# Kernel tuning notes

Hardware: AMD Instinct MI355X
Metric: run time of the kernel (lower is better)

The kernel has to match this reference:

```python
import jax, jax.numpy as jnp
import numpy as np

B, NB, D, H = 2048, 12, 256, 16
NU, NI, NR = 100000, 100000, 6
EPS = 1e-10


def _lin(k, din, dout):
    k1, k2 = jax.random.split(k)
    s = 1.0 / np.sqrt(din)
    w = jax.random.uniform(k1, (din, dout), minval=-s, maxval=s, dtype=jnp.float32)
    b = jax.random.uniform(k2, (dout,), minval=-s, maxval=s, dtype=jnp.float32)
    return w, b


def setup_inputs() -> dict:
    key = jax.random.key(0)
    ks = jax.random.split(key, 24)
    inp = {}
    inp['iids'] = jax.random.randint(ks[0], (B,), 0, NI)
    inp['i_user_pad'] = jnp.stack([
        jax.random.randint(ks[1], (B, NB), 0, NU),
        jax.random.randint(ks[2], (B, NB), 0, NR)], axis=-1)
    inp['i_item_pad'] = jax.random.randint(ks[3], (B, NB), 0, NI)
    inp['i_item_user_pad'] = jnp.stack([
        jax.random.randint(ks[4], (B, NB, NB), 0, NI),
        jax.random.randint(ks[5], (B, NB, NB), 0, NR)], axis=-1)
    inp['user_table'] = jax.random.normal(ks[6], (NU, D), dtype=jnp.float32) * 0.02
    inp['item_table'] = jax.random.normal(ks[7], (NI, D), dtype=jnp.float32) * 0.02
    inp['rate_table'] = jax.random.normal(ks[8], (NR, D), dtype=jnp.float32) * 0.02
    # g_u: 2D -> D -> D
    inp['g_u_w1'], inp['g_u_b1'] = _lin(ks[9], 2 * D, D)
    inp['g_u_w2'], inp['g_u_b2'] = _lin(ks[10], D, D)
    # item_users_att: 2D -> D -> H
    inp['attu_w1'], inp['attu_b1'] = _lin(ks[11], 2 * D, D)
    inp['attu_w2'], inp['attu_b2'] = _lin(ks[12], D, H)
    # item_users_head: NB*H -> NB*H//2 -> NB
    inp['headu_w1'], inp['headu_b1'] = _lin(ks[13], NB * H, NB * H // 2)
    inp['headu_w2'], inp['headu_b2'] = _lin(ks[14], NB * H // 2, NB)
    # aggre_items: D -> D (+relu)
    inp['aggi_w'], inp['aggi_b'] = _lin(ks[15], D, D)
    # item_items_att: 2D -> D -> H
    inp['attii_w1'], inp['attii_b1'] = _lin(ks[16], 2 * D, D)
    inp['attii_w2'], inp['attii_b2'] = _lin(ks[17], D, H)
    # item_items_head: NB*H -> NB*H//2 -> NB
    inp['headii_w1'], inp['headii_b1'] = _lin(ks[18], NB * H, NB * H // 2)
    inp['headii_w2'], inp['headii_b2'] = _lin(ks[19], NB * H // 2, NB)
    # aggre_item2item: D -> D (+relu)
    inp['aggii_w'], inp['aggii_b'] = _lin(ks[20], D, D)
    # combine_mlp: 2D -> D -> D -> D, relu each
    inp['comb_w1'], inp['comb_b1'] = _lin(ks[21], 2 * D, D)
    inp['comb_w2'], inp['comb_b2'] = _lin(ks[22], D, D)
    inp['comb_w3'], inp['comb_b3'] = _lin(ks[23], D, D)
    return inp


def _mlp(x, w1, b1, w2, b2):
    return jax.nn.relu(x @ w1 + b1) @ w2 + b2


def reference(iids, i_user_pad, i_item_pad, i_item_user_pad,
              user_table, item_table, rate_table,
              g_u_w1, g_u_b1, g_u_w2, g_u_b2,
              attu_w1, attu_b1, attu_w2, attu_b2,
              headu_w1, headu_b1, headu_w2, headu_b2,
              aggi_w, aggi_b,
              attii_w1, attii_b1, attii_w2, attii_b2,
              headii_w1, headii_b1, headii_w2, headii_b2,
              aggii_w, aggii_b,
              comb_w1, comb_b1, comb_w2, comb_b2, comb_w3, comb_b3):
    dt = user_table.dtype
    # ---- stage 1: item <- its users ----
    p_t = user_table[i_user_pad[:, :, 0]]                       # [B,NB,D]
    mask_i = (i_user_pad[:, :, 0] > 0).astype(dt)               # [B,NB]
    er = rate_table[i_user_pad[:, :, 1]]                        # [B,NB,D]
    f_jt = _mlp(jnp.concatenate([p_t, er], -1), g_u_w1, g_u_b1, g_u_w2, g_u_b2)
    q_j = mask_i[:, :, None] * item_table[iids][:, None, :]     # [B,NB,D]
    miu = _mlp(jnp.concatenate([f_jt, q_j], -1), attu_w1, attu_b1, attu_w2, attu_b2)  # [B,NB,H]
    miu = _mlp(miu.reshape(miu.shape[0], -1), headu_w1, headu_b1, headu_w2, headu_b2)  # [B,NB]
    miu = jnp.exp(miu) * mask_i
    miu = miu / (jnp.sum(miu, 1, keepdims=True) + EPS)
    h_jU = jax.nn.relu(jnp.einsum('bn,bnd->bd', miu, f_jt) @ aggi_w + aggi_b)
    # ---- stage 2: neighbor items <- their users ----
    q_a_s = item_table[i_item_user_pad[..., 0]]                 # [B,NB,NB,D]
    mask_s = (i_item_user_pad[..., 0] > 0).astype(dt)           # [B,NB,NB]
    er_s = rate_table[i_item_user_pad[..., 1]]
    x_ia_s = _mlp(jnp.concatenate([q_a_s, er_s], -1), g_u_w1, g_u_b1, g_u_w2, g_u_b2)
    p_i_s = mask_s[..., None] * item_table[i_item_pad][:, :, None, :]
    miu_s = _mlp(jnp.concatenate([x_ia_s, p_i_s], -1), attu_w1, attu_b1, attu_w2, attu_b2)  # [B,NB,NB,H]
    miu_s = _mlp(miu_s.reshape(miu_s.shape[0], miu_s.shape[1], -1),
                 headu_w1, headu_b1, headu_w2, headu_b2)        # [B,NB,NB]
    miu_s = jnp.exp(miu_s) * mask_s
    miu_s = miu_s / (jnp.sum(miu_s, 2, keepdims=True) + EPS)
    h_oU = jax.nn.relu(jnp.einsum('bnm,bnmd->bnd', miu_s, x_ia_s) @ aggi_w + aggi_b)  # [B,NB,D]
    # ---- stage 3: item <- neighbor items ----
    kappa = _mlp(jnp.concatenate([h_oU, item_table[i_item_pad]], -1),
                 attii_w1, attii_b1, attii_w2, attii_b2)        # [B,NB,H]
    kappa = _mlp(kappa.reshape(kappa.shape[0], -1), headii_w1, headii_b1, headii_w2, headii_b2)  # [B,NB]
    mask_su = (i_item_pad > 0).astype(dt)
    kappa = jnp.exp(kappa) * mask_su
    kappa = kappa / (jnp.sum(kappa, 1, keepdims=True) + EPS)
    h_jV = jax.nn.relu(jnp.einsum('bn,bnd->bd', kappa, h_oU) @ aggii_w + aggii_b)
    # ---- combine ----
    h = jnp.concatenate([h_jU, h_jV], 1)
    h = jax.nn.relu(h @ comb_w1 + comb_b1)
    h = jax.nn.relu(h @ comb_w2 + comb_b2)
    return jax.nn.relu(h @ comb_w3 + comb_b3)
```

## Files before the change

### kernel.cpp

```cpp
#include <hip/hip_runtime.h>
#include <cstdint>
#include <cstddef>

typedef short short8 __attribute__((ext_vector_type(8)));
typedef short short4v __attribute__((ext_vector_type(4)));
typedef float f32x4 __attribute__((ext_vector_type(4)));
typedef __bf16 bf16x8 __attribute__((ext_vector_type(8)));

__device__ __forceinline__ unsigned short f2bu(float f) {
  return __builtin_bit_cast(unsigned short, (__bf16)f);
}
__device__ __forceinline__ float b2f(unsigned short h) {
  union { unsigned u; float f; } v; v.u = ((unsigned)h) << 16;
  return v.f;
}

__device__ __forceinline__ f32x4 mfma16(short8 a, short8 b, f32x4 c) {
  return __builtin_amdgcn_mfma_f32_16x16x32_bf16(
      __builtin_bit_cast(bf16x8, a), __builtin_bit_cast(bf16x8, b), c, 0, 0, 0);
}

__global__ void k_cvt(const float* __restrict__ in, short* __restrict__ o, int ntot) {
  int i = (blockIdx.x * 256 + threadIdx.x) * 8;
  if (i >= ntot) return;
  float4 a = *(const float4*)(in + i);
  float4 b = *(const float4*)(in + i + 4);
  short8 v;
  v[0] = (short)f2bu(a.x); v[1] = (short)f2bu(a.y);
  v[2] = (short)f2bu(a.z); v[3] = (short)f2bu(a.w);
  v[4] = (short)f2bu(b.x); v[5] = (short)f2bu(b.y);
  v[6] = (short)f2bu(b.z); v[7] = (short)f2bu(b.w);
  *(short8*)(o + i) = v;
}

__global__ void k_cvt_rows(const float* __restrict__ tab, const int* __restrict__ pairs,
                           short* __restrict__ o, int nrows) {
  int t = blockIdx.x * 256 + threadIdx.x;
  if (t >= nrows * 32) return;
  int row = t >> 5;
  int c8 = (t & 31) << 3;
  int id = pairs[2 * row];
  const float* s = tab + (size_t)id * 256 + c8;
  float4 a = *(const float4*)(s);
  float4 b = *(const float4*)(s + 4);
  short8 v;
  v[0] = (short)f2bu(a.x); v[1] = (short)f2bu(a.y);
  v[2] = (short)f2bu(a.z); v[3] = (short)f2bu(a.w);
  v[4] = (short)f2bu(b.x); v[5] = (short)f2bu(b.y);
  v[6] = (short)f2bu(b.z); v[7] = (short)f2bu(b.w);
  *(short8*)(o + (size_t)row * 256 + c8) = v;
}

struct Prep {
  const float* src[16];
  short* dst[16];
  int K[16], N[16], mode[16];
  int boff[17];
};
__global__ void k_prep(Prep p) {
  int b = blockIdx.x, e = 0;
#pragma unroll
  for (int i = 1; i < 16; ++i) if (b >= p.boff[i]) e = i;
  int t = (b - p.boff[e]) * 256 + threadIdx.x;
  const int K = p.K[e], N = p.N[e];
  if (t >= K * N) return;
  const float* w = p.src[e];
  const int m = p.mode[e];
  if (m == 2) { p.dst[e][t] = (short)f2bu(w[t]); return; }
  if (m == 0) {
    int ks = t >> 13, rem = t & 8191;
    int P = rem >> 3, j = rem & 7;
    int n = P >> 2;
    int kq = ((P & 3) - (n >> 1)) & 3;
    int k = (ks << 5) + (kq << 3) + j;
    p.dst[e][t] = (short)f2bu(w[(size_t)k * 256 + n]);
    return;
  }
  int n = t / K, k = t - n * K;
  p.dst[e][t] = (short)f2bu(w[(size_t)k * N + n]);
}

__global__ void k_rc(const float* __restrict__ rate, const float* __restrict__ w1,
                     float* __restrict__ RC) {
  const int j = blockIdx.x;
  const int n = threadIdx.x;
  float s = 0.f;
  const float* rr = rate + j * 256;
  for (int k = 0; k < 256; ++k)
    s += rr[k] * w1[(size_t)(256 + k) * 256 + n];
  RC[j * 256 + n] = s;
}

__global__ __launch_bounds__(256, 4) void k_qc(
    const int* __restrict__ qid, const short* __restrict__ itembf,
    const short* __restrict__ aw1, float* __restrict__ QC)
{
  const int tid = threadIdx.x;
  const int lane = tid & 63;
  const int wave = tid >> 6;
  const int m0 = (int)blockIdx.x << 6;
  const int l15 = lane & 15;
  const int lq = lane >> 4;
  const int nb = wave << 6;

  int pBg[4];
  const short* qp[4];
#pragma unroll
  for (int i = 0; i < 4; ++i) {
    int n = nb + i * 16 + l15;
    pBg[i] = (n * 4 + ((lq + (n >> 1)) & 3)) * 8;
    qp[i] = itembf + (size_t)qid[m0 + i * 16 + l15] * 256 + lq * 8;
  }

  const f32x4 fz = {0.f, 0.f, 0.f, 0.f};
  f32x4 acc[4][4];
#pragma unroll
  for (int ni = 0; ni < 4; ++ni)
#pragma unroll
    for (int mi = 0; mi < 4; ++mi) acc[ni][mi] = fz;

  for (int ks = 0; ks < 8; ++ks) {
    short8 wf[4], qf[4];
#pragma unroll
    for (int i = 0; i < 4; ++i) {
      wf[i] = *(const short8*)(aw1 + (8 + ks) * 8192 + pBg[i]);
      qf[i] = *(const short8*)(qp[i] + ks * 32);
    }
#pragma unroll
    for (int ni = 0; ni < 4; ++ni)
#pragma unroll
      for (int mi = 0; mi < 4; ++mi)
        acc[ni][mi] = mfma16(wf[ni], qf[mi], acc[ni][mi]);
  }
#pragma unroll
  for (int ni = 0; ni < 4; ++ni) {
    const int nbase = nb + ni * 16 + lq * 4;
#pragma unroll
    for (int mi = 0; mi < 4; ++mi) {
      const int m = mi * 16 + l15;
      *(f32x4*)(QC + (size_t)(m0 + m) * 256 + nbase) = acc[ni][mi];
    }
  }
}

template <bool IDENT>
__global__ __launch_bounds__(256, 3) void k_fused(
    const int* __restrict__ idx_pairs,
    const short* __restrict__ tab0,
    const float* __restrict__ RC,
    const float* __restrict__ QC,
    const short* __restrict__ ws1, const float* __restrict__ b1,
    const short* __restrict__ ws2, const float* __restrict__ b2,
    const short* __restrict__ aw1, const float* __restrict__ ab1,
    const short* __restrict__ aw2t, const float* __restrict__ ab2,
    short* __restrict__ Xout, short* __restrict__ miu_out)
{
  __shared__ __align__(16) short smem[20480];
  short* sA0 = smem;
  short* sA1 = smem + 2048;
  short* sH  = smem + 4096;

  const int tid = threadIdx.x;
  const int lane = tid & 63;
  const int wave = tid >> 6;
  const int m0 = (int)blockIdx.x << 6;
  const int l15 = lane & 15;
  const int lq = lane >> 4;
  const int nb = wave << 6;
  const int swz = (l15 & 7) << 3;

  const int an = tid >> 2;
  const int kqA = ((tid & 3) - (an >> 1)) & 3;
  const int r = m0 + an;
  const int i0 = idx_pairs[2 * r];
  const short* a0 = (IDENT ? (tab0 + (size_t)r * 256) : (tab0 + (size_t)i0 * 256)) + kqA * 8;

  int pBg[4], pA[4];
#pragma unroll
  for (int i = 0; i < 4; ++i) {
    int n = nb + i * 16 + l15;
    pBg[i] = (n * 4 + ((lq + (n >> 1)) & 3)) * 8;
    int m = i * 16 + l15;
    pA[i] = (m * 4 + ((lq + (m >> 1)) & 3)) * 8;
  }
  const int hOff = lq * 8;

  const f32x4 fz = {0.f, 0.f, 0.f, 0.f};
  f32x4 acc[4][4];
#pragma unroll
  for (int ni = 0; ni < 4; ++ni)
#pragma unroll
    for (int mi = 0; mi < 4; ++mi) acc[ni][mi] = fz;

  short8 wfb[3][4];
  short8 ar0, ar1;

  int i1v[4], mskv[4], grpv[4];
#pragma unroll
  for (int mi = 0; mi < 4; ++mi) {
    const int row = m0 + mi * 16 + l15;
    i1v[mi]  = idx_pairs[2 * row + 1];
    mskv[mi] = idx_pairs[2 * row];
    grpv[mi] = row / 12;
  }

  {
    short8 t = *(const short8*)a0;
    *(short8*)(sA0 + tid * 8) = t;
  }
  ar1 = *(const short8*)(a0 + 32);
#pragma unroll
  for (int i = 0; i < 4; ++i) wfb[0][i] = *(const short8*)(ws1 + pBg[i]);
#pragma unroll
  for (int i = 0; i < 4; ++i) wfb[1][i] = *(const short8*)(ws1 + 8192 + pBg[i]);
  __syncthreads();
#pragma unroll
  for (int ks = 0; ks < 8; ++ks) {
    short* sAc = (ks & 1) ? sA1 : sA0;
    short* sAn = (ks & 1) ? sA0 : sA1;
    if (ks < 6) {
      const int c = ks + 2;
      short8 t = *(const short8*)(a0 + c * 32);
      if ((ks & 1) == 0) ar0 = t; else ar1 = t;
      const short* s = ws1 + c * 8192;
#pragma unroll
      for (int i = 0; i < 4; ++i) wfb[c % 3][i] = *(const short8*)(s + pBg[i]);
    }
    short8 xf[4];
#pragma unroll
    for (int i = 0; i < 4; ++i) xf[i] = *(short8*)(sAc + pA[i]);
#pragma unroll
    for (int ni = 0; ni < 4; ++ni)
#pragma unroll
      for (int mi = 0; mi < 4; ++mi)
        acc[ni][mi] = mfma16(wfb[ks % 3][ni], xf[mi], acc[ni][mi]);
    if (ks < 7) {
      short8 w = (((ks + 1) & 1) == 0) ? ar0 : ar1;
      *(short8*)(sAn + tid * 8) = w;
      __syncthreads();
    }
  }
#pragma unroll
  for (int ni = 0; ni < 4; ++ni) {
    const int nbase = nb + ni * 16 + lq * 4;
    float4 bb = *(const float4*)(b1 + nbase);
#pragma unroll
    for (int mi = 0; mi < 4; ++mi) {
      const int m = mi * 16 + l15;
      float4 rc = *(const float4*)(RC + i1v[mi] * 256 + nbase);
      short4v hv;
      hv[0] = (short)f2bu(fmaxf(acc[ni][mi][0] + rc.x + bb.x, 0.f));
      hv[1] = (short)f2bu(fmaxf(acc[ni][mi][1] + rc.y + bb.y, 0.f));
      hv[2] = (short)f2bu(fmaxf(acc[ni][mi][2] + rc.z + bb.z, 0.f));
      hv[3] = (short)f2bu(fmaxf(acc[ni][mi][3] + rc.w + bb.w, 0.f));
      *(short4v*)(sH + m * 256 + (nbase ^ swz)) = hv;
    }
  }
  __syncthreads();

#pragma unroll
  for (int ni = 0; ni < 4; ++ni)
#pragma unroll
    for (int mi = 0; mi < 4; ++mi) acc[ni][mi] = fz;
#pragma unroll
  for (int i = 0; i < 4; ++i) wfb[0][i] = *(const short8*)(ws2 + pBg[i]);
#pragma unroll
  for (int i = 0; i < 4; ++i) wfb[1][i] = *(const short8*)(ws2 + 8192 + pBg[i]);
#pragma unroll
  for (int ks = 0; ks < 8; ++ks) {
    if (ks < 6) {
      const short* s = ws2 + (ks + 2) * 8192;
#pragma unroll
      for (int i = 0; i < 4; ++i) wfb[(ks + 2) % 3][i] = *(const short8*)(s + pBg[i]);
    }
    short8 hf[4];
#pragma unroll
    for (int i = 0; i < 4; ++i)
      hf[i] = *(short8*)(sH + (i * 16 + l15) * 256 + ((ks * 32 + hOff) ^ swz));
#pragma unroll
    for (int ni = 0; ni < 4; ++ni)
#pragma unroll
      for (int mi = 0; mi < 4; ++mi)
        acc[ni][mi] = mfma16(wfb[ks % 3][ni], hf[mi], acc[ni][mi]);
  }
  __syncthreads();

#pragma unroll
  for (int ni = 0; ni < 4; ++ni) {
    const int nbase = nb + ni * 16 + lq * 4;
    float4 bb = *(const float4*)(b2 + nbase);
#pragma unroll
    for (int mi = 0; mi < 4; ++mi) {
      const int m = mi * 16 + l15;
      short4v hv;
      hv[0] = (short)f2bu(acc[ni][mi][0] + bb.x);
      hv[1] = (short)f2bu(acc[ni][mi][1] + bb.y);
      hv[2] = (short)f2bu(acc[ni][mi][2] + bb.z);
      hv[3] = (short)f2bu(acc[ni][mi][3] + bb.w);
      *(short4v*)(sH + m * 256 + (nbase ^ swz)) = hv;
    }
  }
  __syncthreads();

#pragma unroll
  for (int p = 0; p < 8; ++p) {
    const int rr = (tid >> 5) + p * 8;
    const int c8 = (tid & 31) * 8;
    short8 v = *(short8*)(sH + rr * 256 + (c8 ^ ((rr & 7) << 3)));
    *(short8*)(Xout + (size_t)(m0 + rr) * 256 + c8) = v;
  }

#pragma unroll
  for (int ni = 0; ni < 4; ++ni)
#pragma unroll
    for (int mi = 0; mi < 4; ++mi) acc[ni][mi] = fz;
#pragma unroll
  for (int i = 0; i < 4; ++i) wfb[0][i] = *(const short8*)(aw1 + pBg[i]);
#pragma unroll
  for (int i = 0; i < 4; ++i) wfb[1][i] = *(const short8*)(aw1 + 8192 + pBg[i]);
#pragma unroll
  for (int ks = 0; ks < 8; ++ks) {
    if (ks < 6) {
      const short* s = aw1 + (ks + 2) * 8192;
#pragma unroll
      for (int i = 0; i < 4; ++i) wfb[(ks + 2) % 3][i] = *(const short8*)(s + pBg[i]);
    }
    short8 xf[4];
#pragma unroll
    for (int i = 0; i < 4; ++i)
      xf[i] = *(short8*)(sH + (i * 16 + l15) * 256 + ((ks * 32 + hOff) ^ swz));
#pragma unroll
    for (int ni = 0; ni < 4; ++ni)
#pragma unroll
      for (int mi = 0; mi < 4; ++mi)
        acc[ni][mi] = mfma16(wfb[ks % 3][ni], xf[mi], acc[ni][mi]);
  }
  __syncthreads();

#pragma unroll
  for (int ni = 0; ni < 4; ++ni) {
    const int nbase = nb + ni * 16 + lq * 4;
    float4 bb = *(const float4*)(ab1 + nbase);
#pragma unroll
    for (int mi = 0; mi < 4; ++mi) {
      const int m = mi * 16 + l15;
      float4 qv;
      if (mskv[mi] > 0) qv = *(const float4*)(QC + (size_t)grpv[mi] * 256 + nbase);
      else { qv.x = 0.f; qv.y = 0.f; qv.z = 0.f; qv.w = 0.f; }
      short4v hv;
      hv[0] = (short)f2bu(fmaxf(acc[ni][mi][0] + qv.x + bb.x, 0.f));
      hv[1] = (short)f2bu(fmaxf(acc[ni][mi][1] + qv.y + bb.y, 0.f));
      hv[2] = (short)f2bu(fmaxf(acc[ni][mi][2] + qv.z + bb.z, 0.f));
      hv[3] = (short)f2bu(fmaxf(acc[ni][mi][3] + qv.w + bb.w, 0.f));
      *(short4v*)(sH + m * 256 + (nbase ^ swz)) = hv;
    }
  }
  __syncthreads();

  f32x4 a2 = fz;
#pragma unroll
  for (int ks = 0; ks < 8; ++ks) {
    short8 af = *(short8*)(sH + (wave * 16 + l15) * 256 + ((ks * 32 + hOff) ^ swz));
    short8 bv = *(const short8*)(aw2t + l15 * 256 + ks * 32 + hOff);
    a2 = mfma16(af, bv, a2);
  }
  const float bias = ab2[l15];
#pragma unroll
  for (int j = 0; j < 4; ++j)
    miu_out[(size_t)(m0 + wave * 16 + lq * 4 + j) * 16 + l15] = (short)f2bu(a2[j] + bias);
}

__global__ __launch_bounds__(256, 3) void k_attonly(
    const short* __restrict__ first,
    const short* __restrict__ itembf,
    const int* __restrict__ iidx,
    const short* __restrict__ aw1, const float* __restrict__ ab1,
    const short* __restrict__ aw2t, const float* __restrict__ ab2,
    short* __restrict__ out)
{
  __shared__ __align__(16) short sH[16896];

  const int tid = threadIdx.x;
  const int lane = tid & 63;
  const int wave = tid >> 6;
  const int m0 = (int)blockIdx.x << 6;
  const int l15 = lane & 15;
  const int lq = lane >> 4;
  const int nb = wave << 6;
  const int hOff = lq * 8;

  const short* fp[4];
  const short* qp[4];
  int pBg[4];
#pragma unroll
  for (int i = 0; i < 4; ++i) {
    int mrow = m0 + i * 16 + l15;
    fp[i] = first + (size_t)mrow * 256 + hOff;
    qp[i] = itembf + (size_t)iidx[mrow] * 256 + hOff;
    int n = nb + i * 16 + l15;
    pBg[i] = (n * 4 + ((lq + (n >> 1)) & 3)) * 8;
  }

  const f32x4 fz = {0.f, 0.f, 0.f, 0.f};
  f32x4 acc[4][4];
#pragma unroll
  for (int ni = 0; ni < 4; ++ni)
#pragma unroll
    for (int mi = 0; mi < 4; ++mi) acc[ni][mi] = fz;

  short8 wfc[4], wfn[4], xfc[4], xfn[4];
#pragma unroll
  for (int i = 0; i < 4; ++i) {
    wfc[i] = *(const short8*)(aw1 + pBg[i]);
    xfc[i] = *(const short8*)(fp[i]);
  }
  for (int ks = 0; ks < 16; ++ks) {
    if (ks < 15) {
      const int c = ks + 1;
      const short* s = aw1 + c * 8192;
#pragma unroll
      for (int i = 0; i < 4; ++i) {
        wfn[i] = *(const short8*)(s + pBg[i]);
        xfn[i] = *(const short8*)((c < 8) ? (fp[i] + c * 32) : (qp[i] + (c - 8) * 32));
      }
    }
#pragma unroll
    for (int ni = 0; ni < 4; ++ni)
#pragma unroll
      for (int mi = 0; mi < 4; ++mi)
        acc[ni][mi] = mfma16(wfc[ni], xfc[mi], acc[ni][mi]);
    if (ks < 15) {
#pragma unroll
      for (int i = 0; i < 4; ++i) { wfc[i] = wfn[i]; xfc[i] = xfn[i]; }
    }
  }
#pragma unroll
  for (int ni = 0; ni < 4; ++ni) {
    const int nbase = nb + ni * 16 + lq * 4;
    float4 bb = *(const float4*)(ab1 + nbase);
#pragma unroll
    for (int mi = 0; mi < 4; ++mi) {
      const int m = mi * 16 + l15;
      short4v hv;
      hv[0] = (short)f2bu(fmaxf(acc[ni][mi][0] + bb.x, 0.f));
      hv[1] = (short)f2bu(fmaxf(acc[ni][mi][1] + bb.y, 0.f));
      hv[2] = (short)f2bu(fmaxf(acc[ni][mi][2] + bb.z, 0.f));
      hv[3] = (short)f2bu(fmaxf(acc[ni][mi][3] + bb.w, 0.f));
      *(short4v*)(sH + m * 264 + nbase) = hv;
    }
  }
  __syncthreads();
  f32x4 a2 = fz;
#pragma unroll
  for (int ks = 0; ks < 8; ++ks) {
    short8 af = *(short8*)(sH + (wave * 16 + l15) * 264 + ks * 32 + hOff);
    short8 bv = *(const short8*)(aw2t + l15 * 256 + ks * 32 + hOff);
    a2 = mfma16(af, bv, a2);
  }
  const float bias = ab2[l15];
#pragma unroll
  for (int j = 0; j < 4; ++j)
    out[(size_t)(m0 + wave * 16 + lq * 4 + j) * 16 + l15] = (short)f2bu(a2[j] + bias);
}

__global__ __launch_bounds__(256, 3) void k_gemm1(
    const short* __restrict__ Abf, const short* __restrict__ wt,
    const float* __restrict__ bias, short* __restrict__ out)
{
  const int tid  = threadIdx.x;
  const int lane = tid & 63;
  const int wave = tid >> 6;
  const int m0   = blockIdx.x << 6;
  const int l15  = lane & 15;
  const int lq   = lane >> 4;
  const int rq   = lq << 2;
  const int nb   = wave << 6;
  const int hOff = lq * 8;

  const f32x4 fz = {0.f, 0.f, 0.f, 0.f};
  f32x4 acc[4][4];
#pragma unroll
  for (int mi = 0; mi < 4; ++mi)
#pragma unroll
    for (int ni = 0; ni < 4; ++ni) acc[mi][ni] = fz;

  for (int ks = 0; ks < 8; ++ks) {
    short8 af[4], bv[4];
#pragma unroll
    for (int i = 0; i < 4; ++i) {
      af[i] = *(const short8*)(Abf + (size_t)(m0 + i * 16 + l15) * 256 + ks * 32 + hOff);
      bv[i] = *(const short8*)(wt + (size_t)(nb + i * 16 + l15) * 256 + ks * 32 + hOff);
    }
#pragma unroll
    for (int mi = 0; mi < 4; ++mi)
#pragma unroll
      for (int ni = 0; ni < 4; ++ni)
        acc[mi][ni] = mfma16(af[mi], bv[ni], acc[mi][ni]);
  }

#pragma unroll
  for (int ni = 0; ni < 4; ++ni) {
    const int col = nb + ni * 16 + l15;
    const float b = bias[col];
#pragma unroll
    for (int mi = 0; mi < 4; ++mi)
#pragma unroll
      for (int j = 0; j < 4; ++j) {
        const int row = mi * 16 + rq + j;
        out[(size_t)(m0 + row) * 256 + col] = (short)f2bu(fmaxf(acc[mi][ni][j] + b, 0.f));
      }
  }
}

__global__ __launch_bounds__(256, 2) void k_comb(
    const short* __restrict__ hju, const short* __restrict__ hjv,
    const short* __restrict__ w1t, const float* __restrict__ b1,
    const short* __restrict__ w2t, const float* __restrict__ b2,
    const short* __restrict__ w3t, const float* __restrict__ b3,
    float* __restrict__ out)
{
  __shared__ __align__(16) short smem[29696];
  short (*A)[40]   = (short(*)[40])smem;
  short (*Bt)[40]  = (short(*)[40])(smem + 2560);
  short (*Hh)[264] = (short(*)[264])(smem + 12800);

  const int tid  = threadIdx.x;
  const int lane = tid & 63;
  const int wave = tid >> 6;
  const int m0   = blockIdx.x << 6;
  const int arow = tid >> 2;
  const int acol8 = (tid & 3) << 3;
  const int lrow = lane & 15;
  const int lk8  = (lane >> 4) << 3;
  const int rq   = (lane >> 4) << 2;
  const int nb   = wave << 6;
  const int r = m0 + arow;

  const f32x4 fz = {0.f, 0.f, 0.f, 0.f};
  f32x4 acc[4][4];
#pragma unroll
  for (int mi = 0; mi < 4; ++mi)
#pragma unroll
    for (int ni = 0; ni < 4; ++ni) acc[mi][ni] = fz;

  for (int ks = 0; ks < 16; ++ks) {
    const int kg = (ks << 5) + acol8;
    short8 av = (kg < 256) ? *(const short8*)(hju + (size_t)r * 256 + kg)
                           : *(const short8*)(hjv + (size_t)r * 256 + (kg - 256));
    *(short8*)&A[arow][acol8] = av;
    const short* wsrc = w1t + tid * 512 + (ks << 5);
    *(short8*)&Bt[tid][0]  = *(const short8*)(wsrc);
    *(short8*)&Bt[tid][8]  = *(const short8*)(wsrc + 8);
    *(short8*)&Bt[tid][16] = *(const short8*)(wsrc + 16);
    *(short8*)&Bt[tid][24] = *(const short8*)(wsrc + 24);
    __syncthreads();
    short8 af[4], bv[4];
#pragma unroll
    for (int mi = 0; mi < 4; ++mi) af[mi] = *(short8*)&A[mi * 16 + lrow][lk8];
#pragma unroll
    for (int ni = 0; ni < 4; ++ni) bv[ni] = *(short8*)&Bt[nb + ni * 16 + lrow][lk8];
#pragma unroll
    for (int mi = 0; mi < 4; ++mi)
#pragma unroll
      for (int ni = 0; ni < 4; ++ni)
        acc[mi][ni] = mfma16(af[mi], bv[ni], acc[mi][ni]);
    __syncthreads();
  }
#pragma unroll
  for (int ni = 0; ni < 4; ++ni) {
    const int col = nb + ni * 16 + lrow;
    const float bias = b1[col];
#pragma unroll
    for (int mi = 0; mi < 4; ++mi)
#pragma unroll
      for (int j = 0; j < 4; ++j)
        Hh[mi * 16 + rq + j][col] = (short)f2bu(fmaxf(acc[mi][ni][j] + bias, 0.f));
  }

#pragma unroll
  for (int mi = 0; mi < 4; ++mi)
#pragma unroll
    for (int ni = 0; ni < 4; ++ni) acc[mi][ni] = fz;
  for (int ks = 0; ks < 8; ++ks) {
    const short* wsrc = w2t + tid * 256 + (ks << 5);
    *(short8*)&Bt[tid][0]  = *(const short8*)(wsrc);
    *(short8*)&Bt[tid][8]  = *(const short8*)(wsrc + 8);
    *(short8*)&Bt[tid][16] = *(const short8*)(wsrc + 16);
    *(short8*)&Bt[tid][24] = *(const short8*)(wsrc + 24);
    __syncthreads();
    short8 af[4], bv[4];
#pragma unroll
    for (int mi = 0; mi < 4; ++mi) af[mi] = *(short8*)&Hh[mi * 16 + lrow][(ks << 5) + lk8];
#pragma unroll
    for (int ni = 0; ni < 4; ++ni) bv[ni] = *(short8*)&Bt[nb + ni * 16 + lrow][lk8];
#pragma unroll
    for (int mi = 0; mi < 4; ++mi)
#pragma unroll
      for (int ni = 0; ni < 4; ++ni)
        acc[mi][ni] = mfma16(af[mi], bv[ni], acc[mi][ni]);
    __syncthreads();
  }
#pragma unroll
  for (int ni = 0; ni < 4; ++ni) {
    const int col = nb + ni * 16 + lrow;
    const float bias = b2[col];
#pragma unroll
    for (int mi = 0; mi < 4; ++mi)
#pragma unroll
      for (int j = 0; j < 4; ++j)
        Hh[mi * 16 + rq + j][col] = (short)f2bu(fmaxf(acc[mi][ni][j] + bias, 0.f));
  }
  __syncthreads();

#pragma unroll
  for (int mi = 0; mi < 4; ++mi)
#pragma unroll
    for (int ni = 0; ni < 4; ++ni) acc[mi][ni] = fz;
  for (int ks = 0; ks < 8; ++ks) {
    const short* wsrc = w3t + tid * 256 + (ks << 5);
    *(short8*)&Bt[tid][0]  = *(const short8*)(wsrc);
    *(short8*)&Bt[tid][8]  = *(const short8*)(wsrc + 8);
    *(short8*)&Bt[tid][16] = *(const short8*)(wsrc + 16);
    *(short8*)&Bt[tid][24] = *(const short8*)(wsrc + 24);
    __syncthreads();
    short8 af[4], bv[4];
#pragma unroll
    for (int mi = 0; mi < 4; ++mi) af[mi] = *(short8*)&Hh[mi * 16 + lrow][(ks << 5) + lk8];
#pragma unroll
    for (int ni = 0; ni < 4; ++ni) bv[ni] = *(short8*)&Bt[nb + ni * 16 + lrow][lk8];
#pragma unroll
    for (int mi = 0; mi < 4; ++mi)
#pragma unroll
      for (int ni = 0; ni < 4; ++ni)
        acc[mi][ni] = mfma16(af[mi], bv[ni], acc[mi][ni]);
    __syncthreads();
  }
#pragma unroll
  for (int ni = 0; ni < 4; ++ni) {
    const int col = nb + ni * 16 + lrow;
    const float bias = b3[col];
#pragma unroll
    for (int mi = 0; mi < 4; ++mi)
#pragma unroll
      for (int j = 0; j < 4; ++j) {
        const int row = mi * 16 + rq + j;
        out[(size_t)(m0 + row) * 256 + col] = fmaxf(acc[mi][ni][j] + bias, 0.f);
      }
  }
}

__global__ __launch_bounds__(256, 4) void k_h1(
    const short* __restrict__ A, const short* __restrict__ w1t,
    const float* __restrict__ b1, short* __restrict__ h1)
{
  const int tid = threadIdx.x;
  const int lane = tid & 63;
  const int wave = tid >> 6;
  const int m0 = (int)blockIdx.x << 6;
  const int l15 = lane & 15;
  const int lq = lane >> 4;
  const int ntc = (wave < 2) ? 2 : 1;
  const int nta = wave;
  const int ntb = wave + 4;

  const f32x4 fz = {0.f, 0.f, 0.f, 0.f};
  f32x4 acc[4][2];
#pragma unroll
  for (int i = 0; i < 4; ++i) { acc[i][0] = fz; acc[i][1] = fz; }

  for (int ks = 0; ks < 6; ++ks) {
    short8 af[4], bv[2];
#pragma unroll
    for (int i = 0; i < 4; ++i)
      af[i] = *(const short8*)(A + (size_t)(m0 + i * 16 + l15) * 192 + ks * 32 + lq * 8);
    bv[0] = *(const short8*)(w1t + (nta * 16 + l15) * 192 + ks * 32 + lq * 8);
    if (ntc == 2)
      bv[1] = *(const short8*)(w1t + (ntb * 16 + l15) * 192 + ks * 32 + lq * 8);
#pragma unroll
    for (int j = 0; j < 2; ++j)
      if (j < ntc)
#pragma unroll
        for (int i = 0; i < 4; ++i)
          acc[i][j] = mfma16(bv[j], af[i], acc[i][j]);
  }
#pragma unroll
  for (int j = 0; j < 2; ++j) {
    if (j >= ntc) continue;
    const int nbase = (j == 0 ? nta : ntb) * 16 + lq * 4;
    float4 bb = *(const float4*)(b1 + nbase);
#pragma unroll
    for (int i = 0; i < 4; ++i) {
      const int row = m0 + i * 16 + l15;
      short4v hv;
      hv[0] = (short)f2bu(fmaxf(acc[i][j][0] + bb.x, 0.f));
      hv[1] = (short)f2bu(fmaxf(acc[i][j][1] + bb.y, 0.f));
      hv[2] = (short)f2bu(fmaxf(acc[i][j][2] + bb.z, 0.f));
      hv[3] = (short)f2bu(fmaxf(acc[i][j][3] + bb.w, 0.f));
      *(short4v*)(h1 + (size_t)row * 96 + nbase) = hv;
    }
  }
}

__global__ __launch_bounds__(256) void k_h2(
    const short* __restrict__ h1, const short* __restrict__ w2t,
    const float* __restrict__ b2,
    const int* __restrict__ mask_src, const int mstride,
    float* __restrict__ W)
{
  __shared__ float wgt[16][12];
  const int tid = threadIdx.x;
  const int gg = tid >> 4, sl = tid & 15;
  const int g = blockIdx.x * 16 + gg;
  if (sl < 12) {
    float s = b2[sl];
    const short* hr = h1 + (size_t)g * 96;
    const short* wr = w2t + sl * 96;
#pragma unroll
    for (int kk = 0; kk < 12; ++kk) {
      short8 hv = *(const short8*)(hr + kk * 8);
      short8 wv = *(const short8*)(wr + kk * 8);
#pragma unroll
      for (int j = 0; j < 8; ++j)
        s += b2f((unsigned short)hv[j]) * b2f((unsigned short)wv[j]);
    }
    const int mi = mask_src[(g * 12 + sl) * mstride];
    wgt[gg][sl] = (mi > 0) ? expf(s) : 0.f;
  }
  __syncthreads();
  if (sl < 12) {
    float tot = 1e-10f;
#pragma unroll
    for (int m = 0; m < 12; ++m) tot += wgt[gg][m];
    W[(size_t)g * 12 + sl] = wgt[gg][sl] / tot;
  }
}

__global__ __launch_bounds__(256) void k_wsum(
    const float* __restrict__ W, const short* __restrict__ X,
    short* __restrict__ out)
{
  const int tid = threadIdx.x;
  const int g = blockIdx.x * 8 + (tid >> 5);
  const int d0 = (tid & 31) * 8;
  const float* wg = W + (size_t)g * 12;
  float w[12];
#pragma unroll
  for (int m = 0; m < 12; ++m) w[m] = wg[m];
  const short* xp = X + (size_t)g * 12 * 256 + d0;
  float o[8];
#pragma unroll
  for (int j = 0; j < 8; ++j) o[j] = 0.f;
#pragma unroll
  for (int m = 0; m < 12; ++m) {
    short8 x = *(const short8*)(xp + m * 256);
#pragma unroll
    for (int j = 0; j < 8; ++j) o[j] += w[m] * b2f((unsigned short)x[j]);
  }
  short8 v;
#pragma unroll
  for (int j = 0; j < 8; ++j) v[j] = (short)f2bu(o[j]);
  *(short8*)(out + (size_t)g * 256 + d0) = v;
}

extern "C" void kernel_launch(void* const* d_in, const int* in_sizes, int n_in,
                              void* d_out, int out_size, void* d_ws, size_t ws_size,
                              hipStream_t stream)
{
  (void)in_sizes; (void)n_in; (void)out_size; (void)ws_size;

  const int*   iids = (const int*)d_in[0];
  const int*   iup  = (const int*)d_in[1];
  const int*   iip  = (const int*)d_in[2];
  const int*   iiup = (const int*)d_in[3];
  const float* user_table = (const float*)d_in[4];
  const float* item_table = (const float*)d_in[5];
  const float* rate_table = (const float*)d_in[6];
  const float* g_u_w1 = (const float*)d_in[7];   const float* g_u_b1 = (const float*)d_in[8];
  const float* g_u_w2 = (const float*)d_in[9];   const float* g_u_b2 = (const float*)d_in[10];
  const float* attu_w1 = (const float*)d_in[11]; const float* attu_b1 = (const float*)d_in[12];
  const float* attu_w2 = (const float*)d_in[13]; const float* attu_b2 = (const float*)d_in[14];
  const float* headu_w1 = (const float*)d_in[15]; const float* headu_b1 = (const float*)d_in[16];
  const float* headu_w2 = (const float*)d_in[17]; const float* headu_b2 = (const float*)d_in[18];
  const float* aggi_w = (const float*)d_in[19];  const float* aggi_b = (const float*)d_in[20];
  const float* attii_w1 = (const float*)d_in[21]; const float* attii_b1 = (const float*)d_in[22];
  const float* attii_w2 = (const float*)d_in[23]; const float* attii_b2 = (const float*)d_in[24];
  const float* headii_w1 = (const float*)d_in[25]; const float* headii_b1 = (const float*)d_in[26];
  const float* headii_w2 = (const float*)d_in[27]; const float* headii_b2 = (const float*)d_in[28];
  const float* aggii_w = (const float*)d_in[29]; const float* aggii_b = (const float*)d_in[30];
  const float* comb_w1 = (const float*)d_in[31]; const float* comb_b1 = (const float*)d_in[32];
  const float* comb_w2 = (const float*)d_in[33]; const float* comb_b2 = (const float*)d_in[34];
  const float* comb_w3 = (const float*)d_in[35]; const float* comb_b3 = (const float*)d_in[36];

  const int NIe = 100000 * 256;
  const int M2 = 2048 * 12 * 12;
  const int M1 = 2048 * 12;
  const int G2 = M1;
  const int G1 = 2048;

  char* wsp = (char*)d_ws;
  size_t off = 0;
  auto alloc = [&](size_t bytes) -> void* {
    void* p = wsp + off;
    off += (bytes + 255) & ~(size_t)255;
    return p;
  };
  short* item_bf = (short*)alloc((size_t)NIe * 2);
  short* urows   = (short*)alloc((size_t)M1 * 256 * 2);
  short* sl_gu1   = (short*)alloc((size_t)512 * 256 * 2);
  short* sl_gu2   = (short*)alloc((size_t)256 * 256 * 2);
  short* sl_attu1 = (short*)alloc((size_t)512 * 256 * 2);
  short* sl_attii1= (short*)alloc((size_t)512 * 256 * 2);
  short* wt_attu2 = (short*)alloc((size_t)256 * 16 * 2);
  short* wt_attii2= (short*)alloc((size_t)256 * 16 * 2);
  short* wt_aggi   = (short*)alloc((size_t)256 * 256 * 2);
  short* wt_aggii  = (short*)alloc((size_t)256 * 256 * 2);
  short* wt_comb1  = (short*)alloc((size_t)512 * 256 * 2);
  short* wt_comb2  = (short*)alloc((size_t)256 * 256 * 2);
  short* wt_comb3  = (short*)alloc((size_t)256 * 256 * 2);
  short* hu1t  = (short*)alloc((size_t)96 * 192 * 2);
  short* hu2t  = (short*)alloc((size_t)12 * 96 * 2);
  short* hii1t = (short*)alloc((size_t)96 * 192 * 2);
  short* hii2t = (short*)alloc((size_t)12 * 96 * 2);
  float* RC    = (float*)alloc((size_t)6 * 256 * 4);
  float* QC2   = (float*)alloc((size_t)G2 * 256 * 4);
  float* QC1   = (float*)alloc((size_t)G1 * 256 * 4);

  short* X      = (short*)alloc((size_t)M2 * 256 * 2);
  short* FJT    = (short*)alloc((size_t)M1 * 256 * 2);
  short* MIU2   = (short*)alloc((size_t)M2 * 16 * 2);
  short* MIU1   = (short*)alloc((size_t)M1 * 16 * 2);
  short* KAP    = (short*)alloc((size_t)M1 * 16 * 2);
  short* H1A    = (short*)alloc((size_t)G2 * 96 * 2);
  short* H1K    = (short*)alloc((size_t)G1 * 96 * 2);
  short* H1M    = (short*)alloc((size_t)G1 * 96 * 2);
  float* WA     = (float*)alloc((size_t)G2 * 12 * 4);
  float* WK     = (float*)alloc((size_t)G1 * 12 * 4);
  float* WM     = (float*)alloc((size_t)G1 * 12 * 4);
  short* HPRE2  = (short*)alloc((size_t)M1 * 256 * 2);
  short* HOU    = (short*)alloc((size_t)M1 * 256 * 2);
  short* HPREJV = (short*)alloc((size_t)2048 * 256 * 2);
  short* HPRE1  = (short*)alloc((size_t)2048 * 256 * 2);
  short* HJU    = (short*)alloc((size_t)2048 * 256 * 2);
  short* HJV    = (short*)alloc((size_t)2048 * 256 * 2);

  k_cvt<<<NIe / 8 / 256, 256, 0, stream>>>(item_table, item_bf, NIe);
  k_cvt_rows<<<(M1 * 32) / 256, 256, 0, stream>>>(user_table, iup, urows, M1);
  k_rc<<<6, 256, 0, stream>>>(rate_table, g_u_w1, RC);

  Prep pp;
  int nbk = 0, ei = 0;
  auto addw = [&](const float* s, short* d, int K, int N, int mode) {
    pp.src[ei] = s; pp.dst[ei] = d; pp.K[ei] = K; pp.N[ei] = N; pp.mode[ei] = mode;
    pp.boff[ei] = nbk; nbk += (K * N + 255) / 256; ++ei;
  };
  addw(g_u_w1,   sl_gu1,    512, 256, 0);
  addw(g_u_w2,   sl_gu2,    256, 256, 0);
  addw(attu_w1,  sl_attu1,  512, 256, 0);
  addw(attii_w1, sl_attii1, 512, 256, 0);
  addw(attu_w2,  wt_attu2,  256, 16, 1);
  addw(attii_w2, wt_attii2, 256, 16, 1);
  addw(aggi_w,   wt_aggi,   256, 256, 1);
  addw(aggii_w,  wt_aggii,  256, 256, 1);
  addw(comb_w1,  wt_comb1,  512, 256, 1);
  addw(comb_w2,  wt_comb2,  256, 256, 1);
  addw(comb_w3,  wt_comb3,  256, 256, 1);
  addw(headu_w1,  hu1t,  192, 96, 1);
  addw(headu_w2,  hu2t,  96, 12, 1);
  addw(headii_w1, hii1t, 192, 96, 1);
  addw(headii_w2, hii2t, 96, 12, 1);
  pp.boff[15] = nbk;
  pp.boff[16] = nbk;
  k_prep<<<nbk, 256, 0, stream>>>(pp);

  k_qc<<<G2 / 64, 256, 0, stream>>>(iip, item_bf, sl_attu1, QC2);
  k_qc<<<G1 / 64, 256, 0, stream>>>(iids, item_bf, sl_attu1, QC1);

  k_fused<false><<<M2 / 64, 256, 0, stream>>>(iiup, item_bf, RC, QC2,
                                              sl_gu1, g_u_b1, sl_gu2, g_u_b2,
                                              sl_attu1, attu_b1, wt_attu2, attu_b2,
                                              X, MIU2);
  k_fused<true><<<M1 / 64, 256, 0, stream>>>(iup, urows, RC, QC1,
                                             sl_gu1, g_u_b1, sl_gu2, g_u_b2,
                                             sl_attu1, attu_b1, wt_attu2, attu_b2,
                                             FJT, MIU1);

  k_h1<<<G2 / 64, 256, 0, stream>>>(MIU2, hu1t, headu_b1, H1A);
  k_h2<<<G2 / 16, 256, 0, stream>>>(H1A, hu2t, headu_b2, iiup, 2, WA);
  k_wsum<<<G2 / 8, 256, 0, stream>>>(WA, X, HPRE2);

  k_gemm1<<<M1 / 64, 256, 0, stream>>>(HPRE2, wt_aggi, aggi_b, HOU);
  k_attonly<<<M1 / 64, 256, 0, stream>>>(HOU, item_bf, iip,
                                         sl_attii1, attii_b1, wt_attii2, attii_b2, KAP);

  k_h1<<<G1 / 64, 256, 0, stream>>>(KAP, hii1t, headii_b1, H1K);
  k_h2<<<G1 / 16, 256, 0, stream>>>(H1K, hii2t, headii_b2, iip, 1, WK);
  k_wsum<<<G1 / 8, 256, 0, stream>>>(WK, HOU, HPREJV);

  k_h1<<<G1 / 64, 256, 0, stream>>>(MIU1, hu1t, headu_b1, H1M);
  k_h2<<<G1 / 16, 256, 0, stream>>>(H1M, hu2t, headu_b2, iup, 2, WM);
  k_wsum<<<G1 / 8, 256, 0, stream>>>(WM, FJT, HPRE1);

  k_gemm1<<<2048 / 64, 256, 0, stream>>>(HPRE1, wt_aggi, aggi_b, HJU);
  k_gemm1<<<2048 / 64, 256, 0, stream>>>(HPREJV, wt_aggii, aggii_b, HJV);
  k_comb<<<2048 / 64, 256, 0, stream>>>(HJU, HJV, wt_comb1, comb_b1,
                                        wt_comb2, comb_b2, wt_comb3, comb_b3,
                                        (float*)d_out);
}
```

Baseline: 484.5 us.

## Merge independent branch launches into combined grouped kernels

Pairs of independent launches (qc, fused, h1, h2, wsum, gemm1 for the user and item-user branches) are merged into single grids, where the block index picks which operand set a block uses. This removes several kernel launches and tail-effect gaps, especially for the small G1-sized grids that underfill the device. The IDENT template becomes a runtime branch, which may add a little register pressure or code overhead in the fused kernel.

```diff
diff --git a/kernel.cpp b/kernel.cpp
--- a/kernel.cpp
+++ b/kernel.cpp
@@ -92,13 +92,20 @@
 }
 
 __global__ __launch_bounds__(256, 4) void k_qc(
-    const int* __restrict__ qid, const short* __restrict__ itembf,
-    const short* __restrict__ aw1, float* __restrict__ QC)
+    int nbA,
+    const int* __restrict__ qidA, float* __restrict__ QCA,
+    const int* __restrict__ qidB, float* __restrict__ QCB,
+    const short* __restrict__ itembf, const short* __restrict__ aw1)
 {
+  int bid = blockIdx.x;
+  const int* qid; float* QC;
+  if (bid < nbA) { qid = qidA; QC = QCA; }
+  else { bid -= nbA; qid = qidB; QC = QCB; }
+
   const int tid = threadIdx.x;
   const int lane = tid & 63;
   const int wave = tid >> 6;
-  const int m0 = (int)blockIdx.x << 6;
+  const int m0 = bid << 6;
   const int l15 = lane & 15;
   const int lq = lane >> 4;
   const int nb = wave << 6;
@@ -143,27 +150,37 @@
   }
 }
 
-template <bool IDENT>
 __global__ __launch_bounds__(256, 3) void k_fused(
-    const int* __restrict__ idx_pairs,
-    const short* __restrict__ tab0,
+    int nbA,
+    const int* __restrict__ idxA, const short* __restrict__ tabA,
+    const float* __restrict__ QCa, short* __restrict__ Xa, short* __restrict__ miuA,
+    const int* __restrict__ idxB, const short* __restrict__ tabB,
+    const float* __restrict__ QCb, short* __restrict__ Xb, short* __restrict__ miuB,
     const float* __restrict__ RC,
-    const float* __restrict__ QC,
     const short* __restrict__ ws1, const float* __restrict__ b1,
     const short* __restrict__ ws2, const float* __restrict__ b2,
     const short* __restrict__ aw1, const float* __restrict__ ab1,
-    const short* __restrict__ aw2t, const float* __restrict__ ab2,
-    short* __restrict__ Xout, short* __restrict__ miu_out)
+    const short* __restrict__ aw2t, const float* __restrict__ ab2)
 {
   __shared__ __align__(16) short smem[20480];
   short* sA0 = smem;
   short* sA1 = smem + 2048;
   short* sH  = smem + 4096;
 
+  int bid = blockIdx.x;
+  const int* idx_pairs; const short* tab0; const float* QC;
+  short* Xout; short* miu_out; bool ident;
+  if (bid < nbA) {
+    idx_pairs = idxA; tab0 = tabA; QC = QCa; Xout = Xa; miu_out = miuA; ident = false;
+  } else {
+    bid -= nbA;
+    idx_pairs = idxB; tab0 = tabB; QC = QCb; Xout = Xb; miu_out = miuB; ident = true;
+  }
+
   const int tid = threadIdx.x;
   const int lane = tid & 63;
   const int wave = tid >> 6;
-  const int m0 = (int)blockIdx.x << 6;
+  const int m0 = bid << 6;
   const int l15 = lane & 15;
   const int lq = lane >> 4;
   const int nb = wave << 6;
@@ -173,7 +190,7 @@
   const int kqA = ((tid & 3) - (an >> 1)) & 3;
   const int r = m0 + an;
   const int i0 = idx_pairs[2 * r];
-  const short* a0 = (IDENT ? (tab0 + (size_t)r * 256) : (tab0 + (size_t)i0 * 256)) + kqA * 8;
+  const short* a0 = (ident ? (tab0 + (size_t)r * 256) : (tab0 + (size_t)i0 * 256)) + kqA * 8;
 
   int pBg[4], pA[4];
 #pragma unroll
@@ -464,13 +481,20 @@
 }
 
 __global__ __launch_bounds__(256, 3) void k_gemm1(
-    const short* __restrict__ Abf, const short* __restrict__ wt,
-    const float* __restrict__ bias, short* __restrict__ out)
+    int nbA,
+    const short* __restrict__ Aa, short* __restrict__ outA,
+    const short* __restrict__ Ab, short* __restrict__ outB,
+    const short* __restrict__ wt, const float* __restrict__ bias)
 {
+  int bid = blockIdx.x;
+  const short* Abf; short* out;
+  if (bid < nbA) { Abf = Aa; out = outA; }
+  else { bid -= nbA; Abf = Ab; out = outB; }
+
   const int tid  = threadIdx.x;
   const int lane = tid & 63;
   const int wave = tid >> 6;
-  const int m0   = blockIdx.x << 6;
+  const int m0   = bid << 6;
   const int l15  = lane & 15;
   const int lq   = lane >> 4;
   const int rq   = lq << 2;
@@ -650,13 +674,20 @@
 }
 
 __global__ __launch_bounds__(256, 4) void k_h1(
-    const short* __restrict__ A, const short* __restrict__ w1t,
-    const float* __restrict__ b1, short* __restrict__ h1)
+    int nbA,
+    const short* __restrict__ Aa, short* __restrict__ h1a,
+    const short* __restrict__ Ab, short* __restrict__ h1b,
+    const short* __restrict__ w1t, const float* __restrict__ b1)
 {
+  int bid = blockIdx.x;
+  const short* A; short* h1;
+  if (bid < nbA) { A = Aa; h1 = h1a; }
+  else { bid -= nbA; A = Ab; h1 = h1b; }
+
   const int tid = threadIdx.x;
   const int lane = tid & 63;
   const int wave = tid >> 6;
-  const int m0 = (int)blockIdx.x << 6;
+  const int m0 = bid << 6;
   const int l15 = lane & 15;
   const int lq = lane >> 4;
   const int ntc = (wave < 2) ? 2 : 1;
@@ -702,15 +733,22 @@
 }
 
 __global__ __launch_bounds__(256) void k_h2(
-    const short* __restrict__ h1, const short* __restrict__ w2t,
-    const float* __restrict__ b2,
-    const int* __restrict__ mask_src, const int mstride,
-    float* __restrict__ W)
+    int nbA,
+    const short* __restrict__ h1a, const int* __restrict__ maskA, int strideA,
+    float* __restrict__ Wa,
+    const short* __restrict__ h1b, const int* __restrict__ maskB, int strideB,
+    float* __restrict__ Wb,
+    const short* __restrict__ w2t, const float* __restrict__ b2)
 {
   __shared__ float wgt[16][12];
+  int bid = blockIdx.x;
+  const short* h1; const int* mask_src; int mstride; float* W;
+  if (bid < nbA) { h1 = h1a; mask_src = maskA; mstride = strideA; W = Wa; }
+  else { bid -= nbA; h1 = h1b; mask_src = maskB; mstride = strideB; W = Wb; }
+
   const int tid = threadIdx.x;
   const int gg = tid >> 4, sl = tid & 15;
-  const int g = blockIdx.x * 16 + gg;
+  const int g = bid * 16 + gg;
   if (sl < 12) {
     float s = b2[sl];
     const short* hr = h1 + (size_t)g * 96;
@@ -736,11 +774,17 @@
 }
 
 __global__ __launch_bounds__(256) void k_wsum(
-    const float* __restrict__ W, const short* __restrict__ X,
-    short* __restrict__ out)
+    int nbA,
+    const float* __restrict__ Wa, const short* __restrict__ Xa, short* __restrict__ outA,
+    const float* __restrict__ Wb, const short* __restrict__ Xb, short* __restrict__ outB)
 {
+  int bid = blockIdx.x;
+  const float* W; const short* X; short* out;
+  if (bid < nbA) { W = Wa; X = Xa; out = outA; }
+  else { bid -= nbA; W = Wb; X = Xb; out = outB; }
+
   const int tid = threadIdx.x;
-  const int g = blockIdx.x * 8 + (tid >> 5);
+  const int g = bid * 8 + (tid >> 5);
   const int d0 = (tid & 31) * 8;
   const float* wg = W + (size_t)g * 12;
   float w[12];
@@ -872,36 +916,35 @@
   pp.boff[16] = nbk;
   k_prep<<<nbk, 256, 0, stream>>>(pp);
 
-  k_qc<<<G2 / 64, 256, 0, stream>>>(iip, item_bf, sl_attu1, QC2);
-  k_qc<<<G1 / 64, 256, 0, stream>>>(iids, item_bf, sl_attu1, QC1);
-
-  k_fused<false><<<M2 / 64, 256, 0, stream>>>(iiup, item_bf, RC, QC2,
-                                              sl_gu1, g_u_b1, sl_gu2, g_u_b2,
-                                              sl_attu1, attu_b1, wt_attu2, attu_b2,
-                                              X, MIU2);
-  k_fused<true><<<M1 / 64, 256, 0, stream>>>(iup, urows, RC, QC1,
-                                             sl_gu1, g_u_b1, sl_gu2, g_u_b2,
-                                             sl_attu1, attu_b1, wt_attu2, attu_b2,
-                                             FJT, MIU1);
-
-  k_h1<<<G2 / 64, 256, 0, stream>>>(MIU2, hu1t, headu_b1, H1A);
-  k_h2<<<G2 / 16, 256, 0, stream>>>(H1A, hu2t, headu_b2, iiup, 2, WA);
-  k_wsum<<<G2 / 8, 256, 0, stream>>>(WA, X, HPRE2);
-
-  k_gemm1<<<M1 / 64, 256, 0, stream>>>(HPRE2, wt_aggi, aggi_b, HOU);
+  k_qc<<<G2 / 64 + G1 / 64, 256, 0, stream>>>(G2 / 64, iip, QC2, iids, QC1,
+                                              item_bf, sl_attu1);
+
+  k_fused<<<M2 / 64 + M1 / 64, 256, 0, stream>>>(
+      M2 / 64,
+      iiup, item_bf, QC2, X, MIU2,
+      iup, urows, QC1, FJT, MIU1,
+      RC, sl_gu1, g_u_b1, sl_gu2, g_u_b2,
+      sl_attu1, attu_b1, wt_attu2, attu_b2);
+
+  k_h1<<<G2 / 64 + G1 / 64, 256, 0, stream>>>(G2 / 64, MIU2, H1A, MIU1, H1M,
+                                              hu1t, headu_b1);
+  k_h2<<<G2 / 16 + G1 / 16, 256, 0, stream>>>(G2 / 16, H1A, iiup, 2, WA,
+                                              H1M, iup, 2, WM, hu2t, headu_b2);
+  k_wsum<<<G2 / 8 + G1 / 8, 256, 0, stream>>>(G2 / 8, WA, X, HPRE2,
+                                              WM, FJT, HPRE1);
+
+  k_gemm1<<<M1 / 64 + G1 / 64, 256, 0, stream>>>(M1 / 64, HPRE2, HOU,
+                                                 HPRE1, HJU, wt_aggi, aggi_b);
+
   k_attonly<<<M1 / 64, 256, 0, stream>>>(HOU, item_bf, iip,
                                          sl_attii1, attii_b1, wt_attii2, attii_b2, KAP);
-
-  k_h1<<<G1 / 64, 256, 0, stream>>>(KAP, hii1t, headii_b1, H1K);
-  k_h2<<<G1 / 16, 256, 0, stream>>>(H1K, hii2t, headii_b2, iip, 1, WK);
-  k_wsum<<<G1 / 8, 256, 0, stream>>>(WK, HOU, HPREJV);
-
-  k_h1<<<G1 / 64, 256, 0, stream>>>(MIU1, hu1t, headu_b1, H1M);
-  k_h2<<<G1 / 16, 256, 0, stream>>>(H1M, hu2t, headu_b2, iup, 2, WM);
-  k_wsum<<<G1 / 8, 256, 0, stream>>>(WM, FJT, HPRE1);
-
-  k_gemm1<<<2048 / 64, 256, 0, stream>>>(HPRE1, wt_aggi, aggi_b, HJU);
-  k_gemm1<<<2048 / 64, 256, 0, stream>>>(HPREJV, wt_aggii, aggii_b, HJV);
+  k_h1<<<G1 / 64, 256, 0, stream>>>(G1 / 64, KAP, H1K, KAP, H1K, hii1t, headii_b1);
+  k_h2<<<G1 / 16, 256, 0, stream>>>(G1 / 16, H1K, iip, 1, WK,
+                                    H1K, iip, 1, WK, hii2t, headii_b2);
+  k_wsum<<<G1 / 8, 256, 0, stream>>>(G1 / 8, WK, HOU, HPREJV, WK, HOU, HPREJV);
+  k_gemm1<<<G1 / 64, 256, 0, stream>>>(G1 / 64, HPREJV, HJV, HPREJV, HJV,
+                                       wt_aggii, aggii_b);
+
   k_comb<<<2048 / 64, 256, 0, stream>>>(HJU, HJV, wt_comb1, comb_b1,
                                         wt_comb2, comb_b2, wt_comb3, comb_b3,
                                         (float*)d_out);
```

Measured after the change: 425.4 us. 12.2% less time.
